# Optimization experiments

Hardware: AMD Instinct MI355X
Metric: run time of the kernel (lower is better)

Reference implementation:

```python
import jax, jax.numpy as jnp
import numpy as np

C_I, C_T, NUM_HEADS = 128, 256, 8
EPS = 1e-5

def conv3d1(x, W, b):
    # 1x1x1 conv: x (b,c,D,H,W), W (o,c), b (o,)
    return jnp.einsum('oc,bcdhw->bodhw', W, x) + b[None, :, None, None, None]

def conv1d1(x, W, b):
    # kernel_size=1 conv: x (b,c,l), W (o,c), b (o,)
    return jnp.einsum('oc,bcl->bol', W, x) + b[None, :, None]

def inorm3d(x):
    # InstanceNorm3d(affine=False): normalize over spatial dims, biased var
    m = jnp.mean(x, axis=(2, 3, 4), keepdims=True)
    v = jnp.var(x, axis=(2, 3, 4), keepdims=True)
    return (x - m) * jax.lax.rsqrt(v + EPS)

def setup_inputs() -> dict:
    key = jax.random.key(0)
    ks = jax.random.split(key, 20)
    B, D, H, W, L = 2, 48, 48, 48, 20
    s = 0.05
    inp = {
        'img_in': jax.random.normal(ks[0], (B, C_I, D, H, W), jnp.float32),
        'lang_in': jax.random.normal(ks[1], (B, C_T, L), jnp.float32),
        'Wq': jax.random.normal(ks[2], (C_I, C_I), jnp.float32) * s,
        'bq': jnp.zeros((C_I,), jnp.float32),
        'Wk': jax.random.normal(ks[3], (C_I, C_T), jnp.float32) * s,
        'bk': jnp.zeros((C_I,), jnp.float32),
        'Wv': jax.random.normal(ks[4], (C_I, C_T), jnp.float32) * s,
        'bv': jnp.zeros((C_I,), jnp.float32),
        'Wpw': jax.random.normal(ks[5], (C_I, C_I), jnp.float32) * s,
        'bpw': jnp.zeros((C_I,), jnp.float32),
        'Wpi': jax.random.normal(ks[6], (C_I, C_I), jnp.float32) * s,
        'bpi': jnp.zeros((C_I,), jnp.float32),
        'Wpo': jax.random.normal(ks[7], (C_I, C_I), jnp.float32) * s,
        'bpo': jnp.zeros((C_I,), jnp.float32),
        'Wg1': jax.random.normal(ks[8], (C_I, C_I), jnp.float32) * s,
        'bg1': jnp.zeros((C_I,), jnp.float32),
        'Wg2': jax.random.normal(ks[9], (C_I, C_I), jnp.float32) * s,
        'bg2': jnp.zeros((C_I,), jnp.float32),
    }
    return inp

def reference(img_in, lang_in, Wq, bq, Wk, bk, Wv, bv, Wpw, bpw, Wpi, bpi,
              Wpo, bpo, Wg1, bg1, Wg2, bg2):
    b = img_in.shape[0]
    d = int(np.prod(img_in.shape[-3:]))
    l = lang_in.shape[-1]
    hd = C_I // NUM_HEADS
    # lang_mask=None path -> all-ones mask (additive term is zero but kept faithful)
    mask = jnp.ones((b, 1, l), img_in.dtype)

    # query: conv3d(1x1)+InstanceNorm -> (b, heads, d, hd)
    q = inorm3d(conv3d1(img_in, Wq, bq)).reshape(b, C_I, d)
    q = q.transpose(0, 2, 1).reshape(b, d, NUM_HEADS, hd).transpose(0, 2, 1, 3)
    # key/value: conv1d(k=1) masked -> (b, heads, hd, l)
    k = (conv1d1(lang_in, Wk, bk) * mask).reshape(b, NUM_HEADS, hd, l)
    v = (conv1d1(lang_in, Wv, bv) * mask).reshape(b, NUM_HEADS, hd, l)

    scale = (C_I / NUM_HEADS) ** (-0.5)
    sim = jnp.einsum('bhdc,bhcl->bhdl', q, k) * scale
    sim = sim + (10000.0 * mask[:, :, None, :] - 10000.0)  # (b,1,1,l) broadcast
    attn = jax.nn.softmax(sim, axis=-1)
    x = jnp.einsum('bhdl,bhcl->bhdc', attn, v)              # (b,heads,d,hd)
    x = x.transpose(0, 2, 1, 3).reshape(b, d, C_I)
    # faithful to torch .permute(0,2,1).permute(0,2,1).view_as(img_in):
    # reshape (b, d, c_i) flat buffer into (b, c_i, D, H, W)
    x_img = x.reshape(img_in.shape)

    skip = inorm3d(conv3d1(img_in, Wpi, bpi))
    weight = inorm3d(conv3d1(x_img, Wpw, bpw))
    out = jax.nn.relu(conv3d1(skip * weight, Wpo, bpo))
    gate = jnp.tanh(conv3d1(jax.nn.relu(conv3d1(out, Wg1, bg1)), Wg2, bg2))
    return out * gate
```

## Files before the change

### kernel.cpp

```cpp
#include <hip/hip_runtime.h>
#include <hip/hip_bf16.h>
#include <cstdint>
#include <cstddef>

#define PSP 110592
#define NCH 128
#define NB  2
#define CPW 68
#define TPB 3
static constexpr float EPSV = 1e-5f;

typedef short bf16x8 __attribute__((ext_vector_type(8)));
typedef float f32x4  __attribute__((ext_vector_type(4)));

static __device__ __forceinline__ uint32_t pk2f(float lo, float hi) {
    __hip_bfloat162 h = __float22bfloat162_rn(make_float2(lo, hi));
    uint32_t u;
    __builtin_memcpy(&u, &h, 4);
    return u;
}
static __device__ __forceinline__ uint32_t pk2s(short lo, short hi) {
    return (uint32_t)(uint16_t)lo | ((uint32_t)(uint16_t)hi << 16);
}
static __device__ __forceinline__ float bf2float(short s) {
    uint32_t u = ((uint32_t)(uint16_t)s) << 16;
    return __builtin_bit_cast(float, u);
}
static __device__ __forceinline__ float bfLO(uint32_t w) {
    return __builtin_bit_cast(float, w << 16);
}
static __device__ __forceinline__ float bfHI(uint32_t w) {
    return __builtin_bit_cast(float, w & 0xffff0000u);
}
static __device__ __forceinline__ int swzb(int p) {
    return (((p & 7) ^ ((p >> 3) & 7)) << 4);
}

__global__ __launch_bounds__(256) void kv_kernel(
    const float* __restrict__ lang,
    const float* __restrict__ Wk, const float* __restrict__ bk,
    const float* __restrict__ Wv, const float* __restrict__ bv,
    float* __restrict__ kout, float* __restrict__ vout)
{
    int gid = blockIdx.x * 256 + threadIdx.x;
    int sel = gid / 5120;
    int r   = gid % 5120;
    int b   = r / 2560;
    int o   = (r % 2560) / 20;
    int l   = r % 20;
    const float* W  = sel ? Wv : Wk;
    const float* bb = sel ? bv : bk;
    const float* lg = lang + b * 256 * 20 + l;
    float acc = bb[o];
    #pragma unroll 8
    for (int c = 0; c < 256; ++c)
        acc = fmaf(W[o * 256 + c], lg[c * 20], acc);
    (sel ? vout : kout)[b * 2560 + o * 20 + l] = acc;
}

__global__ __launch_bounds__(256) void wprep_kernel(
    const float* __restrict__ w0, const float* __restrict__ w1,
    const float* __restrict__ w2, const float* __restrict__ w3,
    const float* __restrict__ w4, const float* __restrict__ w5,
    short* __restrict__ wt)
{
    const int m = blockIdx.x >> 4, s = blockIdx.x & 15;
    const float* src = w0;
    if (m == 1) src = w1; else if (m == 2) src = w2; else if (m == 3) src = w3;
    else if (m == 4) src = w4; else if (m == 5) src = w5;
    short* dst = wt + m * NCH * NCH;
    const int i0 = s * 1024 + threadIdx.x * 4;
    f32x4 v = *(const f32x4*)(src + i0);
    *(uint2*)(dst + i0) = make_uint2(pk2f(v[0], v[1]), pk2f(v[2], v[3]));
}

__global__ __launch_bounds__(256) void knprep_kernel(
    const float* __restrict__ qs, const float* __restrict__ qs2,
    const float* __restrict__ kbuf,
    float* __restrict__ knb, float* __restrict__ cbb)
{
    __shared__ float mq[128], rqs[128], knl[2560];
    const int t = threadIdx.x, b = blockIdx.x;
    if (t < 128) {
        float m = qs[b * 128 + t] * (1.0f / PSP);
        float v = qs2[b * 128 + t] * (1.0f / PSP) - m * m;
        mq[t] = m;
        rqs[t] = rsqrtf(v + EPSV) * 0.25f;
    }
    __syncthreads();
    for (int e = t; e < 2560; e += 256) {
        int c = e / 20;
        float kv = rqs[c] * kbuf[b * 2560 + e];
        knl[e] = kv;
        knb[b * 2560 + e] = kv;
    }
    __syncthreads();
    if (t < 160) {
        int h = t / 20, l = t % 20;
        float s = 0.0f;
        #pragma unroll
        for (int i = 0; i < 16; ++i)
            s = fmaf(mq[h * 16 + i], knl[(h * 16 + i) * 20 + l], s);
        cbb[b * 160 + t] = s;
    }
}

struct PackW { uint32_t lo[8], hi[8]; };

static __device__ __forceinline__ void ldpack_f32(const float* src, PackW& w) {
    const int t = threadIdx.x;
    const float* s = src + (size_t)(4 * (t >> 3)) * PSP + (t & 7) * 8;
    f32x4 r0a = *(const f32x4*)s,             r0b = *(const f32x4*)(s + 4);
    f32x4 r1a = *(const f32x4*)(s + PSP),     r1b = *(const f32x4*)(s + PSP + 4);
    f32x4 r2a = *(const f32x4*)(s + 2 * PSP), r2b = *(const f32x4*)(s + 2 * PSP + 4);
    f32x4 r3a = *(const f32x4*)(s + 3 * PSP), r3b = *(const f32x4*)(s + 3 * PSP + 4);
    #pragma unroll
    for (int j = 0; j < 4; ++j) {
        w.lo[j]     = pk2f(r0a[j], r1a[j]);
        w.lo[4 + j] = pk2f(r0b[j], r1b[j]);
        w.hi[j]     = pk2f(r2a[j], r3a[j]);
        w.hi[4 + j] = pk2f(r2b[j], r3b[j]);
    }
}
static __device__ __forceinline__ void ldpack_b16(const short* src, PackW& w) {
    const int t = threadIdx.x;
    const short* s = src + (size_t)(4 * (t >> 3)) * PSP + (t & 7) * 8;
    bf16x8 r0 = *(const bf16x8*)s;
    bf16x8 r1 = *(const bf16x8*)(s + PSP);
    bf16x8 r2 = *(const bf16x8*)(s + 2 * PSP);
    bf16x8 r3 = *(const bf16x8*)(s + 3 * PSP);
    #pragma unroll
    for (int j = 0; j < 8; ++j) { w.lo[j] = pk2s(r0[j], r1[j]); w.hi[j] = pk2s(r2[j], r3[j]); }
}
static __device__ __forceinline__ void ldpack_g4(const short* skip, const short* wgt,
        const float nm[4][NCH], PackW& w) {
    const int t = threadIdx.x;
    const int c = 4 * (t >> 3), p0 = (t & 7) * 8;
    const short* s = skip + (size_t)c * PSP + p0;
    const short* g = wgt  + (size_t)c * PSP + p0;
    bf16x8 s0 = *(const bf16x8*)s,             s1 = *(const bf16x8*)(s + PSP);
    bf16x8 s2 = *(const bf16x8*)(s + 2 * PSP), s3 = *(const bf16x8*)(s + 3 * PSP);
    bf16x8 g0 = *(const bf16x8*)g,             g1 = *(const bf16x8*)(g + PSP);
    bf16x8 g2 = *(const bf16x8*)(g + 2 * PSP), g3 = *(const bf16x8*)(g + 3 * PSP);
    float mA[4], rA[4], mB[4], rB[4];
    #pragma unroll
    for (int r = 0; r < 4; ++r) {
        mA[r] = nm[0][c + r]; rA[r] = nm[1][c + r];
        mB[r] = nm[2][c + r]; rB[r] = nm[3][c + r];
    }
    #pragma unroll
    for (int j = 0; j < 8; ++j) {
        float v0 = ((bf2float(s0[j]) - mA[0]) * rA[0]) * ((bf2float(g0[j]) - mB[0]) * rB[0]);
        float v1 = ((bf2float(s1[j]) - mA[1]) * rA[1]) * ((bf2float(g1[j]) - mB[1]) * rB[1]);
        float v2 = ((bf2float(s2[j]) - mA[2]) * rA[2]) * ((bf2float(g2[j]) - mB[2]) * rB[2]);
        float v3 = ((bf2float(s3[j]) - mA[3]) * rA[3]) * ((bf2float(g3[j]) - mB[3]) * rB[3]);
        w.lo[j] = pk2f(v0, v1);
        w.hi[j] = pk2f(v2, v3);
    }
}
static __device__ __forceinline__ void stage(char* STGb, const PackW& w) {
    const int t = threadIdx.x;
    const int c8 = (t >> 3) * 8, p0 = (t & 7) * 8;
    #pragma unroll
    for (int j = 0; j < 8; ++j) {
        int byte = (p0 + j) * 256 + c8;
        byte ^= ((j ^ (t & 7)) << 4);
        *(uint2*)(STGb + byte) = make_uint2(w.lo[j], w.hi[j]);
    }
}

static __device__ __forceinline__ void load_afrag16(const short* __restrict__ W16,
                                                    int wid, int lane, bf16x8 af[2][4]) {
    const int orow = wid * 32 + (lane & 15);
    const int cb   = (lane >> 4) * 8;
    #pragma unroll
    for (int mt = 0; mt < 2; ++mt)
        #pragma unroll
        for (int kt = 0; kt < 4; ++kt)
            af[mt][kt] = *(const bf16x8*)(W16 + (size_t)(orow + mt * 16) * NCH + kt * 32 + cb);
}

static __device__ __forceinline__ void run_mfmaX(const char* STGb, const bf16x8 af[2][4],
                                                 f32x4 acc[2][4], int lane) {
    const int l15 = lane & 15, kh = lane >> 4;
    #pragma unroll
    for (int nt = 0; nt < 4; ++nt) {
        const int p = nt * 16 + l15;
        const int sw = swzb(p);
        bf16x8 bf[4];
        #pragma unroll
        for (int kt = 0; kt < 4; ++kt)
            bf[kt] = *(const bf16x8*)(STGb + ((p * 256 + kt * 64 + kh * 16) ^ sw));
        #pragma unroll
        for (int kt = 0; kt < 4; ++kt) {
            acc[0][nt] = __builtin_amdgcn_mfma_f32_16x16x32_bf16(af[0][kt], bf[kt], acc[0][nt], 0, 0, 0);
            acc[1][nt] = __builtin_amdgcn_mfma_f32_16x16x32_bf16(af[1][kt], bf[kt], acc[1][nt], 0, 0, 0);
        }
    }
}
static __device__ __forceinline__ void zero_acc(f32x4 acc[2][4]) {
    #pragma unroll
    for (int m = 0; m < 2; ++m)
        #pragma unroll
        for (int n = 0; n < 4; ++n) acc[m][n] = (f32x4)0.0f;
}
static __device__ __forceinline__ void write_LCp(uint32_t* LCp, const f32x4 acc[2][4],
                                                 int wid, int lane) {
    const int l15 = lane & 15, og = wid * 32 + (lane >> 4) * 4;
    #pragma unroll
    for (int mt = 0; mt < 2; ++mt)
        #pragma unroll
        for (int nt = 0; nt < 4; ++nt) {
            const int o2 = (og >> 1) + mt * 8, p = nt * 16 + l15;
            f32x4 a = acc[mt][nt];
            LCp[o2 * CPW + p]       = pk2f(a[0], a[1]);
            LCp[(o2 + 1) * CPW + p] = pk2f(a[2], a[3]);
        }
}
template<bool RELU, bool STATS>
static __device__ __forceinline__ void epi2(const uint32_t* LCp, const float* __restrict__ bias,
        short* __restrict__ dst, float sS[4], float sQ[4])
{
    const int t = threadIdx.x;
    #pragma unroll
    for (int r = 0; r < 4; ++r) {
        const int u = r * 256 + t, o = u >> 3, ch = u & 7, hi = o & 1;
        const float bia = bias[o];
        const uint32_t* src = LCp + (o >> 1) * CPW + ch * 8;
        uint4 wa = *(const uint4*)src;
        uint4 wb = *(const uint4*)(src + 4);
        uint32_t ww[8] = {wa.x, wa.y, wa.z, wa.w, wb.x, wb.y, wb.z, wb.w};
        float v[8];
        #pragma unroll
        for (int j = 0; j < 8; ++j) v[j] = (hi ? bfHI(ww[j]) : bfLO(ww[j])) + bia;
        if (RELU) {
            #pragma unroll
            for (int j = 0; j < 8; ++j) v[j] = fmaxf(v[j], 0.0f);
        }
        *(uint4*)(dst + (size_t)o * PSP + ch * 8) =
            make_uint4(pk2f(v[0], v[1]), pk2f(v[2], v[3]),
                       pk2f(v[4], v[5]), pk2f(v[6], v[7]));
        if (STATS) {
            float s = 0.0f, q = 0.0f;
            #pragma unroll
            for (int j = 0; j < 8; ++j) { s += v[j]; q += v[j] * v[j]; }
            sS[r] += s; sQ[r] += q;
        }
    }
}
static __device__ __forceinline__ void flush_stats(const float sS[4], const float sQ[4],
        float* __restrict__ s_sum, float* __restrict__ s_sq)
{
    const int t = threadIdx.x;
    #pragma unroll
    for (int r = 0; r < 4; ++r) {
        float s = sS[r], q = sQ[r];
        s += __shfl_xor(s, 1); q += __shfl_xor(q, 1);
        s += __shfl_xor(s, 2); q += __shfl_xor(q, 2);
        s += __shfl_xor(s, 4); q += __shfl_xor(q, 4);
        if ((t & 7) == 0) {
            atomicAdd(&s_sum[r * 32 + (t >> 3)], s);
            atomicAdd(&s_sq [r * 32 + (t >> 3)], q);
        }
    }
}

__global__ __launch_bounds__(256) void g12_kernel(
    const float* __restrict__ img, const short* __restrict__ w16,
    const float* __restrict__ bq, const float* __restrict__ bpi,
    short* __restrict__ qout, short* __restrict__ sout,
    float* __restrict__ qs, float* __restrict__ qs2,
    float* __restrict__ ss, float* __restrict__ ss2)
{
    __shared__ __align__(16) char STGb[16384];
    __shared__ __align__(16) uint32_t LCp[64 * CPW];

    const int t = threadIdx.x, lane = t & 63, wid = t >> 6;
    const int b = blockIdx.y;
    const size_t bbase = (size_t)b * NCH * PSP;
    const int pbase = blockIdx.x * (64 * TPB);
    const int sb = b * NCH;

    bf16x8 afq[2][4], afp[2][4];
    load_afrag16(w16, wid, lane, afq);
    load_afrag16(w16 + NCH * NCH, wid, lane, afp);

    float qS[4] = {0, 0, 0, 0}, qQ[4] = {0, 0, 0, 0};
    float sS[4] = {0, 0, 0, 0}, sQ[4] = {0, 0, 0, 0};

    PackW w;
    ldpack_f32(img + bbase + pbase, w);

    for (int i = 0; i < TPB; ++i) {
        const int pblk = pbase + i * 64;
        stage(STGb, w);
        __syncthreads();
        if (i + 1 < TPB) ldpack_f32(img + bbase + pblk + 64, w);
        f32x4 acc[2][4];
        zero_acc(acc);
        run_mfmaX(STGb, afq, acc, lane);
        write_LCp(LCp, acc, wid, lane);
        __syncthreads();
        epi2<false, true>(LCp, bq, qout + bbase + pblk, qS, qQ);
        zero_acc(acc);
        run_mfmaX(STGb, afp, acc, lane);
        __syncthreads();
        write_LCp(LCp, acc, wid, lane);
        __syncthreads();
        epi2<false, true>(LCp, bpi, sout + bbase + pblk, sS, sQ);
    }
    flush_stats(qS, qQ, qs + sb, qs2 + sb);
    flush_stats(sS, sQ, ss + sb, ss2 + sb);
}

__global__ __launch_bounds__(256) void g3_kernel(
    const short* __restrict__ x, const short* __restrict__ w16,
    const float* __restrict__ bpw, short* __restrict__ wout,
    float* __restrict__ wsu, float* __restrict__ ws2)
{
    __shared__ __align__(16) char STGb[16384];
    __shared__ __align__(16) uint32_t LCp[64 * CPW];

    const int t = threadIdx.x, lane = t & 63, wid = t >> 6;
    const int b = blockIdx.y;
    const size_t bbase = (size_t)b * NCH * PSP;
    const int pbase = blockIdx.x * (64 * TPB);
    const int sb = b * NCH;

    bf16x8 af[2][4];
    load_afrag16(w16, wid, lane, af);
    float wS[4] = {0, 0, 0, 0}, wQ[4] = {0, 0, 0, 0};

    PackW w;
    ldpack_b16(x + bbase + pbase, w);

    for (int i = 0; i < TPB; ++i) {
        const int pblk = pbase + i * 64;
        stage(STGb, w);
        __syncthreads();
        if (i + 1 < TPB) ldpack_b16(x + bbase + pblk + 64, w);
        f32x4 acc[2][4];
        zero_acc(acc);
        run_mfmaX(STGb, af, acc, lane);
        write_LCp(LCp, acc, wid, lane);
        __syncthreads();
        epi2<false, true>(LCp, bpw, wout + bbase + pblk, wS, wQ);
    }
    flush_stats(wS, wQ, wsu + sb, ws2 + sb);
}

__global__ __launch_bounds__(256) void g4_kernel(
    const short* __restrict__ skip, const short* __restrict__ wgt,
    const float* __restrict__ sA, const float* __restrict__ sA2,
    const float* __restrict__ sB, const float* __restrict__ sB2,
    const short* __restrict__ w16, const float* __restrict__ bpo,
    short* __restrict__ outp)
{
    __shared__ __align__(16) char STGb[16384];
    __shared__ __align__(16) uint32_t LCp[64 * CPW];
    __shared__ float nm[4][NCH];

    const int t = threadIdx.x, lane = t & 63, wid = t >> 6;
    const int b = blockIdx.y;
    const size_t bbase = (size_t)b * NCH * PSP;
    const int pbase = blockIdx.x * (64 * TPB);

    if (t < NCH) {
        float m = sA[b * NCH + t] * (1.0f / PSP);
        float v = sA2[b * NCH + t] * (1.0f / PSP) - m * m;
        nm[0][t] = m; nm[1][t] = rsqrtf(v + EPSV);
    } else {
        int c = t - NCH;
        float m = sB[b * NCH + c] * (1.0f / PSP);
        float v = sB2[b * NCH + c] * (1.0f / PSP) - m * m;
        nm[2][c] = m; nm[3][c] = rsqrtf(v + EPSV);
    }
    bf16x8 af[2][4];
    load_afrag16(w16, wid, lane, af);
    __syncthreads();

    PackW w;
    ldpack_g4(skip + bbase + pbase, wgt + bbase + pbase, nm, w);
    float dS[4], dQ[4];

    for (int i = 0; i < TPB; ++i) {
        const int pblk = pbase + i * 64;
        stage(STGb, w);
        __syncthreads();
        if (i + 1 < TPB)
            ldpack_g4(skip + bbase + pblk + 64, wgt + bbase + pblk + 64, nm, w);
        f32x4 acc[2][4];
        zero_acc(acc);
        run_mfmaX(STGb, af, acc, lane);
        write_LCp(LCp, acc, wid, lane);
        __syncthreads();
        epi2<true, false>(LCp, bpo, outp + bbase + pblk, dS, dQ);
    }
}

__global__ __launch_bounds__(256) void g56_kernel(
    const short* __restrict__ outb, const short* __restrict__ w16g1,
    const float* __restrict__ bg1, const short* __restrict__ w16g2,
    const float* __restrict__ bg2, float* __restrict__ fin)
{
    __shared__ __align__(16) char STGb[16384];
    __shared__ __align__(16) char RTL[64 * CPW * 4];

    const int t = threadIdx.x, lane = t & 63, wid = t >> 6;
    const int b = blockIdx.y;
    const size_t bbase = (size_t)b * NCH * PSP;
    const int pbase = blockIdx.x * (64 * TPB);

    bf16x8 af1[2][4], af2[2][4];
    load_afrag16(w16g1, wid, lane, af1);
    load_afrag16(w16g2, wid, lane, af2);

    float bg1v[2][4];
    {
        const int og = wid * 32 + (lane >> 4) * 4;
        #pragma unroll
        for (int mt = 0; mt < 2; ++mt)
            #pragma unroll
            for (int r = 0; r < 4; ++r) bg1v[mt][r] = bg1[og + mt * 16 + r];
    }

    PackW w;
    ldpack_b16(outb + bbase + pbase, w);

    for (int i = 0; i < TPB; ++i) {
        const int pblk = pbase + i * 64;
        stage(STGb, w);
        __syncthreads();
        if (i + 1 < TPB) ldpack_b16(outb + bbase + pblk + 64, w);
        f32x4 acc[2][4];
        zero_acc(acc);
        run_mfmaX(STGb, af1, acc, lane);
        {
            const int l15 = lane & 15, og = wid * 32 + (lane >> 4) * 4;
            #pragma unroll
            for (int mt = 0; mt < 2; ++mt)
                #pragma unroll
                for (int nt = 0; nt < 4; ++nt) {
                    const int o = og + mt * 16, p = nt * 16 + l15;
                    const int sw = swzb(p);
                    f32x4 a = acc[mt][nt];
                    float z0 = fmaxf(a[0] + bg1v[mt][0], 0.0f);
                    float z1 = fmaxf(a[1] + bg1v[mt][1], 0.0f);
                    float z2 = fmaxf(a[2] + bg1v[mt][2], 0.0f);
                    float z3 = fmaxf(a[3] + bg1v[mt][3], 0.0f);
                    *(uint32_t*)(RTL + ((p * 256 + o * 2) ^ sw))     = pk2f(z0, z1);
                    *(uint32_t*)(RTL + ((p * 256 + o * 2 + 4) ^ sw)) = pk2f(z2, z3);
                }
        }
        __syncthreads();
        zero_acc(acc);
        run_mfmaX(RTL, af2, acc, lane);
        __syncthreads();
        write_LCp((uint32_t*)RTL, acc, wid, lane);
        __syncthreads();
        {
            const uint32_t* LCp = (const uint32_t*)RTL;
            float* dst = fin + bbase + pblk;
            #pragma unroll
            for (int r = 0; r < 4; ++r) {
                const int u = r * 256 + t, o2 = u >> 4, ch = u & 15;
                const float b0 = bg2[2 * o2], b1 = bg2[2 * o2 + 1];
                uint4 lc = *(const uint4*)(LCp + o2 * CPW + ch * 4);
                uint32_t lw[4] = {lc.x, lc.y, lc.z, lc.w};
                f32x4 oA, oB;
                #pragma unroll
                for (int j = 0; j < 4; ++j) {
                    const int p = ch * 4 + j;
                    uint32_t mw = *(const uint32_t*)(STGb + ((p * 256 + o2 * 4) ^ swzb(p)));
                    oA[j] = bfLO(mw) * tanhf(bfLO(lw[j]) + b0);
                    oB[j] = bfHI(mw) * tanhf(bfHI(lw[j]) + b1);
                }
                *(f32x4*)(dst + (size_t)(2 * o2) * PSP + ch * 4)     = oA;
                *(f32x4*)(dst + (size_t)(2 * o2 + 1) * PSP + ch * 4) = oB;
            }
        }
        __syncthreads();
    }
}

__global__ __launch_bounds__(256) void attn3_kernel(
    const short* __restrict__ qpre, const float* __restrict__ knb,
    const float* __restrict__ cbb, const float* __restrict__ vbuf,
    short* __restrict__ xout)
{
    __shared__ __align__(16) uint32_t QX[64 * 65];
    __shared__ float KN[2560], VV[2560], CB[160];

    const int t = threadIdx.x;
    const int b = blockIdx.y;
    const int pblk = blockIdx.x * 64;
    const size_t bbase = (size_t)b * NCH * PSP;

    {
        const float* kn = knb + b * 2560;
        const float* vv = vbuf + b * 2560;
        #pragma unroll
        for (int e = t; e < 2560; e += 256) { KN[e] = kn[e]; VV[e] = vv[e]; }
        if (t < 160) CB[t] = cbb[b * 160 + t];
    }
    {
        const int c2 = t >> 2, p0 = (t & 3) * 16;
        const short* s0 = qpre + bbase + (size_t)(2 * c2) * PSP + pblk + p0;
        bf16x8 a0 = *(const bf16x8*)s0,         a1 = *(const bf16x8*)(s0 + 8);
        bf16x8 b0 = *(const bf16x8*)(s0 + PSP), b1 = *(const bf16x8*)(s0 + PSP + 8);
        uint32_t w[16];
        #pragma unroll
        for (int k = 0; k < 8; ++k) { w[k] = pk2s(a0[k], b0[k]); w[8 + k] = pk2s(a1[k], b1[k]); }
        uint32_t* base = QX + c2 * 65 + p0;
        #pragma unroll
        for (int k = 0; k < 8; ++k) *(uint2*)(base + 2 * k) = make_uint2(w[2 * k], w[2 * k + 1]);
    }
    __syncthreads();

    const int p = t & 63, h0 = t >> 6;
    uint32_t qw[16];
    #pragma unroll
    for (int i = 0; i < 8; ++i) {
        qw[i]     = QX[(h0 * 8 + i) * 65 + p];
        qw[8 + i] = QX[((h0 + 4) * 8 + i) * 65 + p];
    }
    __syncthreads();

    #pragma unroll 1
    for (int hh = 0; hh < 2; ++hh) {
        const int h = h0 + hh * 4;
        const int c0 = h * 16;
        float sim[20];
        #pragma unroll
        for (int l = 0; l < 20; ++l) sim[l] = -CB[h * 20 + l];
        #pragma unroll
        for (int i = 0; i < 8; ++i) {
            const uint32_t w = qw[hh * 8 + i];
            const float qlo = bfLO(w), qhi = bfHI(w);
            const float* k0 = KN + (c0 + 2 * i) * 20;
            #pragma unroll
            for (int l = 0; l < 20; ++l)
                sim[l] = fmaf(qlo, k0[l], fmaf(qhi, k0[20 + l], sim[l]));
        }
        float mx = sim[0];
        #pragma unroll
        for (int l = 1; l < 20; ++l) mx = fmaxf(mx, sim[l]);
        float se = 0.0f;
        #pragma unroll
        for (int l = 0; l < 20; ++l) { float e = __expf(sim[l] - mx); sim[l] = e; se += e; }
        const float inv = 1.0f / se;
        #pragma unroll
        for (int i = 0; i < 8; ++i) {
            const float* v0 = VV + (c0 + 2 * i) * 20;
            float x0 = 0.0f, x1 = 0.0f;
            #pragma unroll
            for (int l = 0; l < 20; ++l) {
                x0 = fmaf(sim[l], v0[l], x0);
                x1 = fmaf(sim[l], v0[20 + l], x1);
            }
            QX[p * 65 + h * 8 + i] = pk2f(x0 * inv, x1 * inv);
        }
    }
    __syncthreads();

    {
        const int lane = t & 63, w = t >> 6;
        uint32_t* gdst = (uint32_t*)(xout + bbase + (size_t)pblk * NCH);
        #pragma unroll
        for (int j = 0; j < 4; ++j) {
            const int pp = w * 4 + j * 16 + (lane >> 4);
            const int cw = (lane & 15) * 4;
            const uint32_t* s = QX + pp * 65 + cw;
            *(uint4*)(gdst + pp * 64 + cw) = make_uint4(s[0], s[1], s[2], s[3]);
        }
    }
}

extern "C" void kernel_launch(void* const* d_in, const int* in_sizes, int n_in,
                              void* d_out, int out_size, void* d_ws, size_t ws_size,
                              hipStream_t stream)
{
    const float* img  = (const float*)d_in[0];
    const float* lang = (const float*)d_in[1];
    const float* Wq   = (const float*)d_in[2];
    const float* bq   = (const float*)d_in[3];
    const float* Wk   = (const float*)d_in[4];
    const float* bk   = (const float*)d_in[5];
    const float* Wv   = (const float*)d_in[6];
    const float* bv   = (const float*)d_in[7];
    const float* Wpw  = (const float*)d_in[8];
    const float* bpw  = (const float*)d_in[9];
    const float* Wpi  = (const float*)d_in[10];
    const float* bpi  = (const float*)d_in[11];
    const float* Wpo  = (const float*)d_in[12];
    const float* bpo  = (const float*)d_in[13];
    const float* Wg1  = (const float*)d_in[14];
    const float* bg1  = (const float*)d_in[15];
    const float* Wg2  = (const float*)d_in[16];
    const float* bg2  = (const float*)d_in[17];
    float* outp = (float*)d_out;

    const size_t N = (size_t)NB * NCH * PSP;
    const size_t needed = 3 * N * sizeof(short) + 6 * NCH * NCH * sizeof(short)
                        + (3 * 2 * 2560 + 2 * 160 + 6 * 256) * sizeof(float);
    if (ws_size < needed) return;

    short* bufA = (short*)d_ws;
    short* bufB = bufA + N;
    short* bufC = bufB + N;
    short* wt16 = bufC + N;
    float* kbuf = (float*)(wt16 + 6 * NCH * NCH);
    float* vbuf = kbuf + 2 * 2560;
    float* knb  = vbuf + 2 * 2560;
    float* cbb  = knb + 2 * 2560;
    float* st   = cbb + 2 * 160;
    float* qs   = st;
    float* qs2  = st + 256;
    float* ss   = st + 512;
    float* ss2  = st + 768;
    float* wsu  = st + 1024;
    float* ws2  = st + 1280;

    (void)hipMemsetAsync(st, 0, 6 * 256 * sizeof(float), stream);
    kv_kernel<<<dim3(40), dim3(256), 0, stream>>>(lang, Wk, bk, Wv, bv, kbuf, vbuf);
    wprep_kernel<<<dim3(96), dim3(256), 0, stream>>>(Wq, Wpi, Wpw, Wpo, Wg1, Wg2, wt16);

    const dim3 gg(PSP / (64 * TPB), NB), gb(256);

    g12_kernel<<<gg, gb, 0, stream>>>(img, wt16, bq, bpi, bufA, bufC, qs, qs2, ss, ss2);
    knprep_kernel<<<dim3(NB), dim3(256), 0, stream>>>(qs, qs2, kbuf, knb, cbb);
    attn3_kernel<<<dim3(PSP / 64, NB), gb, 0, stream>>>(bufA, knb, cbb, vbuf, bufB);
    g3_kernel<<<gg, gb, 0, stream>>>(bufB, wt16 + 2 * NCH * NCH, bpw, bufA, wsu, ws2);
    g4_kernel<<<gg, gb, 0, stream>>>(bufC, bufA, ss, ss2, wsu, ws2,
                                     wt16 + 3 * NCH * NCH, bpo, bufB);
    g56_kernel<<<gg, gb, 0, stream>>>(bufB, wt16 + 4 * NCH * NCH, bg1,
                                      wt16 + 5 * NCH * NCH, bg2, outp);
}
```

Measured before the change: 334.1 us.

## Fuse output projection and gating convs into one kernel, raise tiles per block

```diff
diff --git a/kernel.cpp b/kernel.cpp
--- a/kernel.cpp
+++ b/kernel.cpp
@@ -7,7 +7,7 @@
 #define NCH 128
 #define NB  2
 #define CPW 68
-#define TPB 3
+#define TPB 4
 static constexpr float EPSV = 1e-5f;
 
 typedef short bf16x8 __attribute__((ext_vector_type(8)));
@@ -204,6 +204,24 @@
         #pragma unroll
         for (int n = 0; n < 4; ++n) acc[m][n] = (f32x4)0.0f;
 }
+static __device__ __forceinline__ void acc_to_tile(char* dest, const f32x4 acc[2][4],
+        const float bias[2][4], int wid, int lane) {
+    const int l15 = lane & 15, og0 = wid * 32 + (lane >> 4) * 4;
+    #pragma unroll
+    for (int mt = 0; mt < 2; ++mt)
+        #pragma unroll
+        for (int nt = 0; nt < 4; ++nt) {
+            const int o = og0 + mt * 16, p = nt * 16 + l15;
+            const int sw = swzb(p);
+            f32x4 a = acc[mt][nt];
+            float z0 = fmaxf(a[0] + bias[mt][0], 0.0f);
+            float z1 = fmaxf(a[1] + bias[mt][1], 0.0f);
+            float z2 = fmaxf(a[2] + bias[mt][2], 0.0f);
+            float z3 = fmaxf(a[3] + bias[mt][3], 0.0f);
+            *(uint32_t*)(dest + ((p * 256 + o * 2) ^ sw))     = pk2f(z0, z1);
+            *(uint32_t*)(dest + ((p * 256 + o * 2 + 4) ^ sw)) = pk2f(z2, z3);
+        }
+}
 static __device__ __forceinline__ void write_LCp(uint32_t* LCp, const f32x4 acc[2][4],
                                                  int wid, int lane) {
     const int l15 = lane & 15, og = wid * 32 + (lane >> 4) * 4;
@@ -349,15 +367,18 @@
     flush_stats(wS, wQ, wsu + sb, ws2 + sb);
 }
 
-__global__ __launch_bounds__(256) void g4_kernel(
+__global__ __launch_bounds__(256, 3) void g456_kernel(
     const short* __restrict__ skip, const short* __restrict__ wgt,
     const float* __restrict__ sA, const float* __restrict__ sA2,
     const float* __restrict__ sB, const float* __restrict__ sB2,
-    const short* __restrict__ w16, const float* __restrict__ bpo,
-    short* __restrict__ outp)
+    const short* __restrict__ w16po, const float* __restrict__ bpo,
+    const short* __restrict__ w16g1, const float* __restrict__ bg1,
+    const short* __restrict__ w16g2, const float* __restrict__ bg2,
+    float* __restrict__ fin)
 {
     __shared__ __align__(16) char STGb[16384];
-    __shared__ __align__(16) uint32_t LCp[64 * CPW];
+    __shared__ __align__(16) char OUTb[16384];
+    __shared__ __align__(16) char RTL[64 * CPW * 4];
     __shared__ float nm[4][NCH];
 
     const int t = threadIdx.x, lane = t & 63, wid = t >> 6;
@@ -375,13 +396,25 @@
         float v = sB2[b * NCH + c] * (1.0f / PSP) - m * m;
         nm[2][c] = m; nm[3][c] = rsqrtf(v + EPSV);
     }
-    bf16x8 af[2][4];
-    load_afrag16(w16, wid, lane, af);
+
+    bf16x8 afPo[2][4], afG1[2][4], afG2[2][4];
+    load_afrag16(w16po, wid, lane, afPo);
+    load_afrag16(w16g1, wid, lane, afG1);
+    load_afrag16(w16g2, wid, lane, afG2);
+
+    const int og0 = wid * 32 + (lane >> 4) * 4;
+    float bov[2][4], bg1v[2][4];
+    #pragma unroll
+    for (int mt = 0; mt < 2; ++mt)
+        #pragma unroll
+        for (int r = 0; r < 4; ++r) {
+            bov[mt][r]  = bpo[og0 + mt * 16 + r];
+            bg1v[mt][r] = bg1[og0 + mt * 16 + r];
+        }
     __syncthreads();
 
     PackW w;
     ldpack_g4(skip + bbase + pbase, wgt + bbase + pbase, nm, w);
-    float dS[4], dQ[4];
 
     for (int i = 0; i < TPB; ++i) {
         const int pblk = pbase + i * 64;
@@ -391,70 +424,15 @@
             ldpack_g4(skip + bbase + pblk + 64, wgt + bbase + pblk + 64, nm, w);
         f32x4 acc[2][4];
         zero_acc(acc);
-        run_mfmaX(STGb, af, acc, lane);
-        write_LCp(LCp, acc, wid, lane);
-        __syncthreads();
-        epi2<true, false>(LCp, bpo, outp + bbase + pblk, dS, dQ);
-    }
-}
-
-__global__ __launch_bounds__(256) void g56_kernel(
-    const short* __restrict__ outb, const short* __restrict__ w16g1,
-    const float* __restrict__ bg1, const short* __restrict__ w16g2,
-    const float* __restrict__ bg2, float* __restrict__ fin)
-{
-    __shared__ __align__(16) char STGb[16384];
-    __shared__ __align__(16) char RTL[64 * CPW * 4];
-
-    const int t = threadIdx.x, lane = t & 63, wid = t >> 6;
-    const int b = blockIdx.y;
-    const size_t bbase = (size_t)b * NCH * PSP;
-    const int pbase = blockIdx.x * (64 * TPB);
-
-    bf16x8 af1[2][4], af2[2][4];
-    load_afrag16(w16g1, wid, lane, af1);
-    load_afrag16(w16g2, wid, lane, af2);
-
-    float bg1v[2][4];
-    {
-        const int og = wid * 32 + (lane >> 4) * 4;
-        #pragma unroll
-        for (int mt = 0; mt < 2; ++mt)
-            #pragma unroll
-            for (int r = 0; r < 4; ++r) bg1v[mt][r] = bg1[og + mt * 16 + r];
-    }
-
-    PackW w;
-    ldpack_b16(outb + bbase + pbase, w);
-
-    for (int i = 0; i < TPB; ++i) {
-        const int pblk = pbase + i * 64;
-        stage(STGb, w);
-        __syncthreads();
-        if (i + 1 < TPB) ldpack_b16(outb + bbase + pblk + 64, w);
-        f32x4 acc[2][4];
+        run_mfmaX(STGb, afPo, acc, lane);
+        acc_to_tile(OUTb, acc, bov, wid, lane);
+        __syncthreads();
         zero_acc(acc);
-        run_mfmaX(STGb, af1, acc, lane);
-        {
-            const int l15 = lane & 15, og = wid * 32 + (lane >> 4) * 4;
-            #pragma unroll
-            for (int mt = 0; mt < 2; ++mt)
-                #pragma unroll
-                for (int nt = 0; nt < 4; ++nt) {
-                    const int o = og + mt * 16, p = nt * 16 + l15;
-                    const int sw = swzb(p);
-                    f32x4 a = acc[mt][nt];
-                    float z0 = fmaxf(a[0] + bg1v[mt][0], 0.0f);
-                    float z1 = fmaxf(a[1] + bg1v[mt][1], 0.0f);
-                    float z2 = fmaxf(a[2] + bg1v[mt][2], 0.0f);
-                    float z3 = fmaxf(a[3] + bg1v[mt][3], 0.0f);
-                    *(uint32_t*)(RTL + ((p * 256 + o * 2) ^ sw))     = pk2f(z0, z1);
-                    *(uint32_t*)(RTL + ((p * 256 + o * 2 + 4) ^ sw)) = pk2f(z2, z3);
-                }
-        }
+        run_mfmaX(OUTb, afG1, acc, lane);
+        acc_to_tile(RTL, acc, bg1v, wid, lane);
         __syncthreads();
         zero_acc(acc);
-        run_mfmaX(RTL, af2, acc, lane);
+        run_mfmaX(RTL, afG2, acc, lane);
         __syncthreads();
         write_LCp((uint32_t*)RTL, acc, wid, lane);
         __syncthreads();
@@ -471,7 +449,7 @@
                 #pragma unroll
                 for (int j = 0; j < 4; ++j) {
                     const int p = ch * 4 + j;
-                    uint32_t mw = *(const uint32_t*)(STGb + ((p * 256 + o2 * 4) ^ swzb(p)));
+                    uint32_t mw = *(const uint32_t*)(OUTb + ((p * 256 + o2 * 4) ^ swzb(p)));
                     oA[j] = bfLO(mw) * tanhf(bfLO(lw[j]) + b0);
                     oB[j] = bfHI(mw) * tanhf(bfHI(lw[j]) + b1);
                 }
@@ -479,7 +457,6 @@
                 *(f32x4*)(dst + (size_t)(2 * o2 + 1) * PSP + ch * 4) = oB;
             }
         }
-        __syncthreads();
     }
 }
 
@@ -631,8 +608,8 @@
     knprep_kernel<<<dim3(NB), dim3(256), 0, stream>>>(qs, qs2, kbuf, knb, cbb);
     attn3_kernel<<<dim3(PSP / 64, NB), gb, 0, stream>>>(bufA, knb, cbb, vbuf, bufB);
     g3_kernel<<<gg, gb, 0, stream>>>(bufB, wt16 + 2 * NCH * NCH, bpw, bufA, wsu, ws2);
-    g4_kernel<<<gg, gb, 0, stream>>>(bufC, bufA, ss, ss2, wsu, ws2,
-                                     wt16 + 3 * NCH * NCH, bpo, bufB);
-    g56_kernel<<<gg, gb, 0, stream>>>(bufB, wt16 + 4 * NCH * NCH, bg1,
-                                      wt16 + 5 * NCH * NCH, bg2, outp);
-}
+    g456_kernel<<<gg, gb, 0, stream>>>(bufC, bufA, ss, ss2, wsu, ws2,
+                                       wt16 + 3 * NCH * NCH, bpo,
+                                       wt16 + 4 * NCH * NCH, bg1,
+                                       wt16 + 5 * NCH * NCH, bg2, outp);
+}
```

New measurement: 462.1 us. 1.38x slower.
